# Kernel tuning notes

Hardware: AMD Instinct MI355X
Metric: run time of the kernel (lower is better)

Reference implementation:

```python
import jax, jax.numpy as jnp
import numpy as np

B, FIXED_LEN, N_FRAME, MID, P = 4096, 8192, 2112, 264, 88
UNROLLED_ITER = 5


def setup_inputs() -> dict:
    key = jax.random.key(0)
    ks = jax.random.split(key, 8)
    # Fourier weights scaled by 1/FIXED_LEN as in fourier_init
    W_cos = jax.random.normal(ks[0], (N_FRAME, FIXED_LEN), jnp.float32) / FIXED_LEN
    W_sin = jax.random.normal(ks[1], (N_FRAME, FIXED_LEN), jnp.float32) / FIXED_LEN
    # template is |cisoid_dict|^2 >= 0; small positive values keep the unrolled loop stable
    template = jax.random.uniform(ks[2], (N_FRAME, MID), jnp.float32) * 0.01
    return {
        "input_this": jax.random.normal(ks[3], (B, FIXED_LEN), jnp.float32),
        "input_prev": jax.random.normal(ks[4], (B, FIXED_LEN), jnp.float32),
        "W_cos": W_cos,
        "W_sin": W_sin,
        "template": template,
        "W1": jax.random.normal(ks[5], (MID, MID), jnp.float32) * 0.05 + jnp.eye(MID, dtype=jnp.float32),
        "b1": jnp.zeros((MID,), jnp.float32),
        "W2": jax.random.normal(ks[6], (P, MID), jnp.float32) * 0.1,
        "b2": jnp.zeros((P,), jnp.float32),
        "Wout": jax.random.normal(ks[7], (P, P), jnp.float32) * 0.1 + 4.0 * jnp.eye(P, dtype=jnp.float32),
        "bout": jnp.full((P,), -3.0, jnp.float32),
    }


def reference(input_this, input_prev, W_cos, W_sin, template, W1, b1, W2, b2, Wout, bout):
    fixed_len = jnp.asarray(input_this.shape[1], input_this.dtype)
    # get_feat: normalized power spectrum features
    n_valid = (jnp.count_nonzero(input_this, axis=1) + 1).astype(input_this.dtype)[:, None]
    scale = fixed_len / n_valid                      # [B, 1]
    x_cos = (input_this @ W_cos.T) * scale           # [B, N_FRAME]
    x_sin = (input_this @ W_sin.T) * scale
    feat = x_cos * x_cos + x_sin * x_sin             # [B, N_FRAME]

    # process_feat: unrolled LISTA-style iterations
    running = feat
    xi = -running
    m = jax.nn.relu(-10.0 * (xi @ template))         # [B, MID]
    for _ in range(UNROLLED_ITER - 1):
        xi = 1.6 * ((m @ template.T) - running) + 0.2 * xi
        m = jax.nn.relu(-8.0 * (xi @ template) + 0.2 * m)

    h = jax.nn.relu(jax.nn.relu(m @ W1.T + b1) @ W2.T + b2)  # [B, P]
    return jax.nn.sigmoid(h @ Wout.T + bout)         # velocity_estimate [B, P]
```

## Files before the change

kernel.cpp:

```cpp
#include <hip/hip_runtime.h>
#include <cstdint>
#include <cstddef>

#define B_SZ 4096
#define KLEN 8192
#define NF   2112
#define MID  264
#define PD   88

typedef _Float16 f16;
typedef _Float16 f16x4 __attribute__((ext_vector_type(4)));
typedef _Float16 f16x8 __attribute__((ext_vector_type(8)));
typedef float    f32x4 __attribute__((ext_vector_type(4)));

__device__ __forceinline__ void gl2lds16(const void* g, void* l) {
    __builtin_amdgcn_global_load_lds(
        (const __attribute__((address_space(1))) void*)g,
        (__attribute__((address_space(3))) void*)l, 16, 0, 0);
}

__global__ void k_row_prep(const float* __restrict__ x, f16* __restrict__ xh,
                           float* __restrict__ alpha) {
    const int row = blockIdx.x;
    const float* xr = x + (size_t)row * KLEN;
    f16* xhr = xh + (size_t)row * KLEN;
    int cnt = 0;
    for (int j = threadIdx.x * 4; j < KLEN; j += 256 * 4) {
        float4 v = *(const float4*)(xr + j);
        f16x4 h = { (f16)v.x, (f16)v.y, (f16)v.z, (f16)v.w };
        *(f16x4*)(xhr + j) = h;
        cnt += (v.x != 0.f) + (v.y != 0.f) + (v.z != 0.f) + (v.w != 0.f);
    }
    for (int off = 32; off > 0; off >>= 1) cnt += __shfl_down(cnt, off);
    __shared__ int lsum[4];
    if ((threadIdx.x & 63) == 0) lsum[threadIdx.x >> 6] = cnt;
    __syncthreads();
    if (threadIdx.x == 0)
        alpha[row] = 8.0f / (float)(lsum[0] + lsum[1] + lsum[2] + lsum[3] + 1);
}

__global__ void k_cvt_w2(const float* __restrict__ wc, const float* __restrict__ ws,
                         f16* __restrict__ whc, f16* __restrict__ whs, int n4) {
    const float* w = blockIdx.y ? ws : wc;
    f16* wh = blockIdx.y ? whs : whc;
    for (int i = blockIdx.x * blockDim.x + threadIdx.x; i < n4; i += gridDim.x * blockDim.x) {
        float4 v = ((const float4*)w)[i];
        f16x4 h = { (f16)(v.x * 8192.f), (f16)(v.y * 8192.f),
                    (f16)(v.z * 8192.f), (f16)(v.w * 8192.f) };
        ((f16x4*)wh)[i] = h;
    }
}

__global__ void k_prep_tt(const float* __restrict__ T, f16* __restrict__ tt) {
    __shared__ float tile[32][33];
    const int k0 = blockIdx.x * 32, n0 = blockIdx.y * 32;
    const int tx = threadIdx.x & 31, ty = threadIdx.x >> 5;
    for (int r = ty; r < 32; r += 8) {
        const int k = k0 + r, n = n0 + tx;
        tile[r][tx] = (n < MID) ? T[(size_t)k * MID + n] : 0.f;
    }
    __syncthreads();
    for (int r = ty; r < 32; r += 8) {
        const int n = n0 + r, k = k0 + tx;
        tt[(size_t)n * NF + k] = (f16)tile[tx][r];
    }
}

__global__ void k_gram(const float* __restrict__ T, float* __restrict__ G) {
    __shared__ float Pp[32][64];
    __shared__ float Qq[32][64];
    const int i0 = blockIdx.x * 64, j0 = blockIdx.y * 64;
    const int tx = threadIdx.x & 15, ty = threadIdx.x >> 4;
    float acc[4][4] = {};
    for (int kc = blockIdx.z * 11; kc < (int)blockIdx.z * 11 + 11; ++kc) {
        const int k0 = kc * 32;
        for (int l = threadIdx.x; l < 32 * 64; l += 256) {
            const int kk = l >> 6, cc = l & 63, kr = k0 + kk;
            Pp[kk][cc] = (i0 + cc < MID) ? T[(size_t)kr * MID + i0 + cc] : 0.f;
            Qq[kk][cc] = (j0 + cc < MID) ? T[(size_t)kr * MID + j0 + cc] : 0.f;
        }
        __syncthreads();
        for (int kk = 0; kk < 32; ++kk) {
            float a_[4], b_[4];
#pragma unroll
            for (int u = 0; u < 4; ++u) a_[u] = Pp[kk][tx * 4 + u];
#pragma unroll
            for (int w = 0; w < 4; ++w) b_[w] = Qq[kk][ty * 4 + w];
#pragma unroll
            for (int u = 0; u < 4; ++u)
#pragma unroll
                for (int w = 0; w < 4; ++w) acc[u][w] += a_[u] * b_[w];
        }
        __syncthreads();
    }
    for (int u = 0; u < 4; ++u) {
        const int gi = i0 + tx * 4 + u;
        if (gi >= MID) continue;
        for (int w = 0; w < 4; ++w) {
            const int gj = j0 + ty * 4 + w;
            if (gj < MID) atomicAdd(&G[(size_t)gi * MID + gj], acc[u][w]);
        }
    }
}

__global__ __launch_bounds__(256, 2) void k_fourier(
    const f16* __restrict__ A, const f16* __restrict__ Bc, const f16* __restrict__ Bs,
    const float* __restrict__ alpha, f16* __restrict__ feat) {
    __shared__ __align__(16) f16 As[2][128 * 64];
    __shared__ __align__(16) f16 Bcs[2][64 * 64];
    __shared__ __align__(16) f16 Bss[2][64 * 64];
    const int tid = threadIdx.x, lane = tid & 63, wave = tid >> 6;
    const int wm = wave & 1, wn = wave >> 1;
    const int m0 = blockIdx.y * 128, n0 = blockIdx.x * 64;

    const int srow = tid >> 3;
    const int scol = ((tid & 7) ^ (srow & 7)) << 3;
    const f16* gA  = A  + (size_t)(m0 + srow) * KLEN + scol;
    const f16* gBc = Bc + (size_t)(n0 + srow) * KLEN + scol;
    const f16* gBs = Bs + (size_t)(n0 + srow) * KLEN + scol;

#define STAGE_F(buf, kq)                                                          \
    {                                                                             \
        _Pragma("unroll")                                                         \
        for (int i = 0; i < 4; ++i)                                               \
            gl2lds16(gA + (size_t)(32 * i) * KLEN + (kq),                         \
                     (char*)&As[buf][0] + (tid + 256 * i) * 16);                  \
        _Pragma("unroll")                                                         \
        for (int i = 0; i < 2; ++i)                                               \
            gl2lds16(gBc + (size_t)(32 * i) * KLEN + (kq),                        \
                     (char*)&Bcs[buf][0] + (tid + 256 * i) * 16);                 \
        _Pragma("unroll")                                                         \
        for (int i = 0; i < 2; ++i)                                               \
            gl2lds16(gBs + (size_t)(32 * i) * KLEN + (kq),                        \
                     (char*)&Bss[buf][0] + (tid + 256 * i) * 16);                 \
    }

    f32x4 accC[4][2], accS[4][2];
    const f32x4 z4 = {0.f, 0.f, 0.f, 0.f};
#pragma unroll
    for (int i = 0; i < 4; ++i)
#pragma unroll
        for (int j = 0; j < 2; ++j) { accC[i][j] = z4; accS[i][j] = z4; }

    STAGE_F(0, 0);
    for (int k0 = 0; k0 < KLEN; k0 += 64) {
        const int cur = (k0 >> 6) & 1;
        __syncthreads();
        if (k0 + 64 < KLEN) STAGE_F(cur ^ 1, k0 + 64);
#pragma unroll
        for (int kk = 0; kk < 2; ++kk) {
            const int chunk0 = kk * 4 + (lane >> 4);
            f16x8 af[4], bcf[2], bsf[2];
#pragma unroll
            for (int mt = 0; mt < 4; ++mt) {
                const int r = wm * 64 + mt * 16 + (lane & 15);
                af[mt] = *(const f16x8*)(&As[cur][0] + r * 64 + ((chunk0 ^ (r & 7)) << 3));
            }
#pragma unroll
            for (int nt = 0; nt < 2; ++nt) {
                const int r = wn * 32 + nt * 16 + (lane & 15);
                const int off = r * 64 + ((chunk0 ^ (r & 7)) << 3);
                bcf[nt] = *(const f16x8*)(&Bcs[cur][0] + off);
                bsf[nt] = *(const f16x8*)(&Bss[cur][0] + off);
            }
#pragma unroll
            for (int mt = 0; mt < 4; ++mt)
#pragma unroll
                for (int nt = 0; nt < 2; ++nt) {
                    accC[mt][nt] = __builtin_amdgcn_mfma_f32_16x16x32_f16(af[mt], bcf[nt], accC[mt][nt], 0, 0, 0);
                    accS[mt][nt] = __builtin_amdgcn_mfma_f32_16x16x32_f16(af[mt], bsf[nt], accS[mt][nt], 0, 0, 0);
                }
        }
    }
#undef STAGE_F
#pragma unroll
    for (int mt = 0; mt < 4; ++mt)
#pragma unroll
        for (int reg = 0; reg < 4; ++reg) {
            const int row = m0 + wm * 64 + mt * 16 + ((lane >> 4) << 2) + reg;
            const float al = alpha[row];
#pragma unroll
            for (int nt = 0; nt < 2; ++nt) {
                const int col = n0 + wn * 32 + nt * 16 + (lane & 15);
                const float xc = accC[mt][nt][reg] * al;
                const float xs = accS[mt][nt][reg] * al;
                feat[(size_t)row * NF + col] = (f16)(xc * xc + xs * xs);
            }
        }
}

__global__ __launch_bounds__(256, 2) void k_ggemm(
    const f16* __restrict__ A, const f16* __restrict__ Bt, float* __restrict__ g64) {
    __shared__ __align__(16) f16 As[2][128 * 64];
    __shared__ __align__(16) f16 Bs_[2][64 * 64];
    const int tid = threadIdx.x, lane = tid & 63, wave = tid >> 6;
    const int wm = wave & 1, wn = wave >> 1;
    const int m0 = blockIdx.y * 128, n0 = blockIdx.x * 64;
    const int srow = tid >> 3;
    const int scol = ((tid & 7) ^ (srow & 7)) << 3;
    const f16* gA = A + (size_t)(m0 + srow) * NF + scol;
    const f16* gB = Bt + (size_t)(n0 + srow) * NF + scol;

#define STAGE_G(buf, kq)                                                          \
    {                                                                             \
        _Pragma("unroll")                                                         \
        for (int i = 0; i < 4; ++i)                                               \
            gl2lds16(gA + (size_t)(32 * i) * NF + (kq),                           \
                     (char*)&As[buf][0] + (tid + 256 * i) * 16);                  \
        _Pragma("unroll")                                                         \
        for (int i = 0; i < 2; ++i)                                               \
            gl2lds16(gB + (size_t)(32 * i) * NF + (kq),                           \
                     (char*)&Bs_[buf][0] + (tid + 256 * i) * 16);                 \
    }

    f32x4 acc[4][2];
    const f32x4 z4 = {0.f, 0.f, 0.f, 0.f};
#pragma unroll
    for (int i = 0; i < 4; ++i)
#pragma unroll
        for (int j = 0; j < 2; ++j) acc[i][j] = z4;

    STAGE_G(0, 0);
    for (int k0 = 0; k0 < NF; k0 += 64) {
        const int cur = (k0 >> 6) & 1;
        __syncthreads();
        if (k0 + 64 < NF) STAGE_G(cur ^ 1, k0 + 64);
#pragma unroll
        for (int kk = 0; kk < 2; ++kk) {
            const int chunk0 = kk * 4 + (lane >> 4);
            f16x8 af[4], bf[2];
#pragma unroll
            for (int mt = 0; mt < 4; ++mt) {
                const int r = wm * 64 + mt * 16 + (lane & 15);
                af[mt] = *(const f16x8*)(&As[cur][0] + r * 64 + ((chunk0 ^ (r & 7)) << 3));
            }
#pragma unroll
            for (int nt = 0; nt < 2; ++nt) {
                const int r = wn * 32 + nt * 16 + (lane & 15);
                bf[nt] = *(const f16x8*)(&Bs_[cur][0] + r * 64 + ((chunk0 ^ (r & 7)) << 3));
            }
#pragma unroll
            for (int mt = 0; mt < 4; ++mt)
#pragma unroll
                for (int nt = 0; nt < 2; ++nt)
                    acc[mt][nt] = __builtin_amdgcn_mfma_f32_16x16x32_f16(af[mt], bf[nt], acc[mt][nt], 0, 0, 0);
        }
    }
#undef STAGE_G
#pragma unroll
    for (int mt = 0; mt < 4; ++mt)
#pragma unroll
        for (int reg = 0; reg < 4; ++reg) {
            const int row = m0 + wm * 64 + mt * 16 + ((lane >> 4) << 2) + reg;
#pragma unroll
            for (int nt = 0; nt < 2; ++nt) {
                const int col = n0 + wn * 32 + nt * 16 + (lane & 15);
                if (col < MID) g64[(size_t)row * MID + col] = acc[mt][nt][reg];
            }
        }
}

__global__ __launch_bounds__(320) void k_tail(
    const float* __restrict__ g64, const float* __restrict__ Gm,
    const float* __restrict__ W1, const float* __restrict__ b1,
    const float* __restrict__ W2, const float* __restrict__ b2,
    const float* __restrict__ Wout, const float* __restrict__ bout,
    float* __restrict__ out) {
    __shared__ __align__(16) float m_l[8 * 268];
    __shared__ __align__(16) float h2_l[8 * 92];
    const int t = threadIdx.x;
    const int r0 = blockIdx.x * 8;
    const bool act = (t < 264);
    const int rb = (t & 3) * 2;
    const int cb = (t >> 2) * 4;

    for (int idx = t; idx < 8 * MID; idx += 320) {
        const int r = idx / MID, c = idx - r * MID;
        const float gv = g64[(size_t)r0 * MID + idx] * 0.015625f;
        m_l[r * 268 + c] = fmaxf(10.f * gv, 0.f);
    }
    float gr[2][4], ur[2][4];
    if (act) {
#pragma unroll
        for (int u = 0; u < 2; ++u) {
            const float4 gq = *(const float4*)&g64[(size_t)(r0 + rb + u) * MID + cb];
            gr[u][0] = gq.x * 0.015625f; gr[u][1] = gq.y * 0.015625f;
            gr[u][2] = gq.z * 0.015625f; gr[u][3] = gq.w * 0.015625f;
#pragma unroll
            for (int j = 0; j < 4; ++j) ur[u][j] = -gr[u][j];
        }
    }
    __syncthreads();

    for (int it = 0; it < 4; ++it) {
        float v[2][4];
        if (act) {
#pragma unroll
            for (int u = 0; u < 2; ++u)
#pragma unroll
                for (int j = 0; j < 4; ++j) v[u][j] = 0.f;
            for (int k = 0; k < MID; k += 4) {
                float4 m4[2];
#pragma unroll
                for (int u = 0; u < 2; ++u) m4[u] = *(const float4*)&m_l[(rb + u) * 268 + k];
#pragma unroll
                for (int j = 0; j < 4; ++j) {
                    const float4 gv4 = *(const float4*)&Gm[(size_t)(cb + j) * MID + k];
#pragma unroll
                    for (int u = 0; u < 2; ++u)
                        v[u][j] += m4[u].x * gv4.x + m4[u].y * gv4.y + m4[u].z * gv4.z + m4[u].w * gv4.w;
                }
            }
        }
        __syncthreads();
        if (act) {
#pragma unroll
            for (int u = 0; u < 2; ++u)
#pragma unroll
                for (int j = 0; j < 4; ++j) {
                    const float un = 1.6f * (v[u][j] - gr[u][j]) + 0.2f * ur[u][j];
                    ur[u][j] = un;
                    float* mp = &m_l[(rb + u) * 268 + cb + j];
                    *mp = fmaxf(-8.f * un + 0.2f * (*mp), 0.f);
                }
        }
        __syncthreads();
    }

    {
        float v[2][4];
        if (act) {
#pragma unroll
            for (int u = 0; u < 2; ++u)
#pragma unroll
                for (int j = 0; j < 4; ++j) v[u][j] = 0.f;
            for (int k = 0; k < MID; k += 4) {
                float4 m4[2];
#pragma unroll
                for (int u = 0; u < 2; ++u) m4[u] = *(const float4*)&m_l[(rb + u) * 268 + k];
#pragma unroll
                for (int j = 0; j < 4; ++j) {
                    const float4 wv = *(const float4*)&W1[(size_t)(cb + j) * MID + k];
#pragma unroll
                    for (int u = 0; u < 2; ++u)
                        v[u][j] += m4[u].x * wv.x + m4[u].y * wv.y + m4[u].z * wv.z + m4[u].w * wv.w;
                }
            }
        }
        __syncthreads();
        if (act) {
#pragma unroll
            for (int u = 0; u < 2; ++u)
#pragma unroll
                for (int j = 0; j < 4; ++j)
                    m_l[(rb + u) * 268 + cb + j] = fmaxf(v[u][j] + b1[cb + j], 0.f);
        }
        __syncthreads();
    }

    const bool act2 = (t < 88);
    const int rb2 = (t & 3) * 2, cb2 = (t >> 2) * 4;
    if (act2) {
        float v[2][4];
#pragma unroll
        for (int u = 0; u < 2; ++u)
#pragma unroll
            for (int j = 0; j < 4; ++j) v[u][j] = 0.f;
        for (int k = 0; k < MID; k += 4) {
            float4 m4[2];
#pragma unroll
            for (int u = 0; u < 2; ++u) m4[u] = *(const float4*)&m_l[(rb2 + u) * 268 + k];
#pragma unroll
            for (int j = 0; j < 4; ++j) {
                const float4 wv = *(const float4*)&W2[(size_t)(cb2 + j) * MID + k];
#pragma unroll
                for (int u = 0; u < 2; ++u)
                    v[u][j] += m4[u].x * wv.x + m4[u].y * wv.y + m4[u].z * wv.z + m4[u].w * wv.w;
            }
        }
#pragma unroll
        for (int u = 0; u < 2; ++u)
#pragma unroll
            for (int j = 0; j < 4; ++j)
                h2_l[(rb2 + u) * 92 + cb2 + j] = fmaxf(v[u][j] + b2[cb2 + j], 0.f);
    }
    __syncthreads();
    if (act2) {
        float v[2][4];
#pragma unroll
        for (int u = 0; u < 2; ++u)
#pragma unroll
            for (int j = 0; j < 4; ++j) v[u][j] = 0.f;
        for (int q = 0; q < PD; q += 4) {
            float4 h4[2];
#pragma unroll
            for (int u = 0; u < 2; ++u) h4[u] = *(const float4*)&h2_l[(rb2 + u) * 92 + q];
#pragma unroll
            for (int j = 0; j < 4; ++j) {
                const float4 wv = *(const float4*)&Wout[(size_t)(cb2 + j) * PD + q];
#pragma unroll
                for (int u = 0; u < 2; ++u)
                    v[u][j] += h4[u].x * wv.x + h4[u].y * wv.y + h4[u].z * wv.z + h4[u].w * wv.w;
            }
        }
#pragma unroll
        for (int u = 0; u < 2; ++u) {
            float4 o;
            o.x = 1.f / (1.f + expf(-(v[u][0] + bout[cb2 + 0])));
            o.y = 1.f / (1.f + expf(-(v[u][1] + bout[cb2 + 1])));
            o.z = 1.f / (1.f + expf(-(v[u][2] + bout[cb2 + 2])));
            o.w = 1.f / (1.f + expf(-(v[u][3] + bout[cb2 + 3])));
            *(float4*)&out[(size_t)(r0 + rb2 + u) * PD + cb2] = o;
        }
    }
}

extern "C" void kernel_launch(void* const* d_in, const int* in_sizes, int n_in,
                              void* d_out, int out_size, void* d_ws, size_t ws_size,
                              hipStream_t stream) {
    (void)in_sizes; (void)n_in; (void)out_size; (void)ws_size;
    const float* inp  = (const float*)d_in[0];
    const float* wcos = (const float*)d_in[2];
    const float* wsin = (const float*)d_in[3];
    const float* tmpl = (const float*)d_in[4];
    const float* W1   = (const float*)d_in[5];
    const float* b1   = (const float*)d_in[6];
    const float* W2   = (const float*)d_in[7];
    const float* b2   = (const float*)d_in[8];
    const float* Wout = (const float*)d_in[9];
    const float* bout = (const float*)d_in[10];
    float* out = (float*)d_out;

    char* p = (char*)d_ws;
    f16* a_h    = (f16*)p;   p += (size_t)B_SZ * KLEN * 2;
    f16* wc_h   = (f16*)p;   p += (size_t)NF * KLEN * 2;
    f16* ws_h   = (f16*)p;   p += (size_t)NF * KLEN * 2;
    f16* feat_h = (f16*)p;   p += (size_t)B_SZ * NF * 2;
    f16* tt_h   = (f16*)p;   p += (size_t)320 * NF * 2;
    float* alpha= (float*)p; p += (size_t)B_SZ * 4;
    float* g64  = (float*)p; p += (size_t)B_SZ * MID * 4;
    float* Gm   = (float*)p; p += (size_t)MID * MID * 4;

    hipMemsetAsync(Gm, 0, (size_t)MID * MID * 4, stream);
    k_row_prep<<<B_SZ, 256, 0, stream>>>(inp, a_h, alpha);
    k_cvt_w2<<<dim3(2048, 2), 256, 0, stream>>>(wcos, wsin, wc_h, ws_h,
                                                (int)((size_t)NF * KLEN / 4));
    k_prep_tt<<<dim3(NF / 32, 10), 256, 0, stream>>>(tmpl, tt_h);
    k_gram<<<dim3(5, 5, 6), 256, 0, stream>>>(tmpl, Gm);
    k_fourier<<<dim3(NF / 64, B_SZ / 128), 256, 0, stream>>>(a_h, wc_h, ws_h, alpha, feat_h);
    k_ggemm<<<dim3(5, B_SZ / 128), 256, 0, stream>>>(feat_h, tt_h, g64);
    k_tail<<<B_SZ / 8, 320, 0, stream>>>(g64, Gm, W1, b1, W2, b2, Wout, bout, out);
}
```

Before: 1.041 ms.

## Single-buffer Fourier GEMM LDS for higher occupancy and swizzle block order

Drops double buffering in the Fourier GEMM, halving LDS per block, and raises launch bounds from 2 to 4 blocks per SM so more waves can hide global-to-LDS latency. It also remaps the linear block id with a stride-8 swizzle so blocks running at the same time share A and B tiles in L2. The trade is that loads and MFMA no longer overlap within a block and each k-step now needs two barriers. Overlap has to come from other resident blocks, and the tighter register limit may cause spills.

```diff
diff --git a/kernel.cpp b/kernel.cpp
--- a/kernel.cpp
+++ b/kernel.cpp
@@ -103,15 +103,19 @@
     }
 }
 
-__global__ __launch_bounds__(256, 2) void k_fourier(
+__global__ __launch_bounds__(256, 4) void k_fourier(
     const f16* __restrict__ A, const f16* __restrict__ Bc, const f16* __restrict__ Bs,
     const float* __restrict__ alpha, f16* __restrict__ feat) {
-    __shared__ __align__(16) f16 As[2][128 * 64];
-    __shared__ __align__(16) f16 Bcs[2][64 * 64];
-    __shared__ __align__(16) f16 Bss[2][64 * 64];
+    __shared__ __align__(16) f16 As[128 * 64];
+    __shared__ __align__(16) f16 Bcs[64 * 64];
+    __shared__ __align__(16) f16 Bss[64 * 64];
     const int tid = threadIdx.x, lane = tid & 63, wave = tid >> 6;
     const int wm = wave & 1, wn = wave >> 1;
-    const int m0 = blockIdx.y * 128, n0 = blockIdx.x * 64;
+
+    const int bid = blockIdx.y * 33 + blockIdx.x;
+    const int swz = (bid & 7) * 132 + (bid >> 3);
+    const int bx = swz % 33, by = swz / 33;
+    const int m0 = by * 128, n0 = bx * 64;
 
     const int srow = tid >> 3;
     const int scol = ((tid & 7) ^ (srow & 7)) << 3;
@@ -119,20 +123,20 @@
     const f16* gBc = Bc + (size_t)(n0 + srow) * KLEN + scol;
     const f16* gBs = Bs + (size_t)(n0 + srow) * KLEN + scol;
 
-#define STAGE_F(buf, kq)                                                          \
+#define STAGE_F(kq)                                                               \
     {                                                                             \
         _Pragma("unroll")                                                         \
         for (int i = 0; i < 4; ++i)                                               \
             gl2lds16(gA + (size_t)(32 * i) * KLEN + (kq),                         \
-                     (char*)&As[buf][0] + (tid + 256 * i) * 16);                  \
+                     (char*)&As[0] + (tid + 256 * i) * 16);                       \
         _Pragma("unroll")                                                         \
         for (int i = 0; i < 2; ++i)                                               \
             gl2lds16(gBc + (size_t)(32 * i) * KLEN + (kq),                        \
-                     (char*)&Bcs[buf][0] + (tid + 256 * i) * 16);                 \
+                     (char*)&Bcs[0] + (tid + 256 * i) * 16);                      \
         _Pragma("unroll")                                                         \
         for (int i = 0; i < 2; ++i)                                               \
             gl2lds16(gBs + (size_t)(32 * i) * KLEN + (kq),                        \
-                     (char*)&Bss[buf][0] + (tid + 256 * i) * 16);                 \
+                     (char*)&Bss[0] + (tid + 256 * i) * 16);                      \
     }
 
     f32x4 accC[4][2], accS[4][2];
@@ -142,11 +146,10 @@
 #pragma unroll
         for (int j = 0; j < 2; ++j) { accC[i][j] = z4; accS[i][j] = z4; }
 
-    STAGE_F(0, 0);
     for (int k0 = 0; k0 < KLEN; k0 += 64) {
-        const int cur = (k0 >> 6) & 1;
-        __syncthreads();
-        if (k0 + 64 < KLEN) STAGE_F(cur ^ 1, k0 + 64);
+        if (k0) __syncthreads();
+        STAGE_F(k0);
+        __syncthreads();
 #pragma unroll
         for (int kk = 0; kk < 2; ++kk) {
             const int chunk0 = kk * 4 + (lane >> 4);
@@ -154,14 +157,14 @@
 #pragma unroll
             for (int mt = 0; mt < 4; ++mt) {
                 const int r = wm * 64 + mt * 16 + (lane & 15);
-                af[mt] = *(const f16x8*)(&As[cur][0] + r * 64 + ((chunk0 ^ (r & 7)) << 3));
+                af[mt] = *(const f16x8*)(&As[0] + r * 64 + ((chunk0 ^ (r & 7)) << 3));
             }
 #pragma unroll
             for (int nt = 0; nt < 2; ++nt) {
                 const int r = wn * 32 + nt * 16 + (lane & 15);
                 const int off = r * 64 + ((chunk0 ^ (r & 7)) << 3);
-                bcf[nt] = *(const f16x8*)(&Bcs[cur][0] + off);
-                bsf[nt] = *(const f16x8*)(&Bss[cur][0] + off);
+                bcf[nt] = *(const f16x8*)(&Bcs[0] + off);
+                bsf[nt] = *(const f16x8*)(&Bss[0] + off);
             }
 #pragma unroll
             for (int mt = 0; mt < 4; ++mt)
```

Result: faster. 958.4 us (-7.9%).
